# Performance work log

Measured on AMD Instinct MI355X. Metric: run time of the kernel, lower is better.

The kernel has to match this reference:

```python
import jax, jax.numpy as jnp
import numpy as np

T, B, D, H = 512, 64, 256, 512


def _linear_params(key, fan_in, fan_out, dtype=jnp.float32):
    # torch nn.Linear default init: U(-1/sqrt(fan_in), 1/sqrt(fan_in))
    k1, k2 = jax.random.split(key)
    bound = 1.0 / np.sqrt(fan_in)
    W = jax.random.uniform(k1, (fan_out, fan_in), dtype, -bound, bound)
    b = jax.random.uniform(k2, (fan_out,), dtype, -bound, bound)
    return W, b


def setup_inputs() -> dict:
    key = jax.random.key(0)
    kx, kf, ki, kg, ko = jax.random.split(key, 5)
    inputs = jax.random.normal(kx, (T, B, D), dtype=jnp.float32)
    Wf, bf = _linear_params(kf, D + H, H)
    Wi, bi = _linear_params(ki, D + H, H)
    Wg, bg = _linear_params(kg, D + H, H)
    Wo, bo = _linear_params(ko, D + H, H)
    return {"inputs": inputs, "Wf": Wf, "bf": bf, "Wi": Wi, "bi": bi,
            "Wg": Wg, "bg": bg, "Wo": Wo, "bo": bo}


def reference(inputs, Wf, bf, Wi, bi, Wg, bg, Wo, bo):
    # inputs: [T, B, D]; gate weights: [H, D+H]; biases: [H]
    batch = inputs.shape[1]
    hidden = Wf.shape[0]
    h0 = jnp.zeros((batch, hidden), dtype=inputs.dtype)
    c0 = jnp.zeros((batch, hidden), dtype=inputs.dtype)

    # Stack the 4 gate linears into one GEMM per step (same math).
    W_all = jnp.concatenate([Wf, Wi, Wg, Wo], axis=0)   # [4H, D+H]
    b_all = jnp.concatenate([bf, bi, bg, bo], axis=0)   # [4H]

    def step(carry, x):
        hx, cx = carry
        combined = jnp.concatenate([x, hx], axis=1)     # [B, D+H]
        gates = combined @ W_all.T + b_all              # [B, 4H]
        f, i, g, o = jnp.split(gates, 4, axis=1)
        f = jax.nn.sigmoid(f)
        i = jax.nn.sigmoid(i)
        g = jnp.tanh(g)
        o = jax.nn.sigmoid(o)
        cx = f * cx + i * g
        hx = o * jnp.tanh(cx)
        return (hx, cx), hx

    (hx, cx), outputs = jax.lax.scan(step, (h0, c0), inputs)
    return outputs, hx, cx
```

## Files before the change

kernel.cpp:

```cpp
#include <hip/hip_runtime.h>

static constexpr int T_STEPS = 512;
static constexpr int BATCH   = 64;
static constexpr int DIN     = 256;
static constexpr int HID     = 512;
static constexpr int KDIM    = DIN + HID;
static constexpr int S4      = 193;
static constexpr int NBLK    = 256;
static constexpr int NPROD   = 64;

__device__ __forceinline__ float fast_sigmoid(float v) {
    return 1.0f / (1.0f + __expf(-v));
}
__device__ __forceinline__ float fast_tanh(float v) {
    return 1.0f - 2.0f / (__expf(2.0f * v) + 1.0f);
}

__device__ __forceinline__ void store_bypass(float* p, float v) {
    __hip_atomic_store((unsigned int*)p, __float_as_uint(v),
                       __ATOMIC_RELAXED, __HIP_MEMORY_SCOPE_AGENT);
}
__device__ __forceinline__ float load_bypass(const float* p) {
    return __uint_as_float(__hip_atomic_load((const unsigned int*)p,
                           __ATOMIC_RELAXED, __HIP_MEMORY_SCOPE_AGENT));
}
__device__ __forceinline__ void store_flag(unsigned* p, unsigned v) {
    __hip_atomic_store(p, v, __ATOMIC_RELAXED, __HIP_MEMORY_SCOPE_AGENT);
}
__device__ __forceinline__ unsigned load_flag(const unsigned* p) {
    return __hip_atomic_load(p, __ATOMIC_RELAXED, __HIP_MEMORY_SCOPE_AGENT);
}

#define DPP_ADD(v, ctrl)                                                  \
    (v) += __uint_as_float(__builtin_amdgcn_update_dpp(                   \
        0u, __float_as_uint(v), (ctrl), 0xF, 0xF, true))

__global__ __launch_bounds__(512, 1)
void lstm_persistent(const float* __restrict__ x,
                     const float* __restrict__ Wf, const float* __restrict__ bfp,
                     const float* __restrict__ Wi, const float* __restrict__ bip,
                     const float* __restrict__ Wg, const float* __restrict__ bgp,
                     const float* __restrict__ Wo, const float* __restrict__ bop,
                     float* __restrict__ out, unsigned* __restrict__ flag_ws) {
    __shared__ float4 W4[32 * S4];
    __shared__ float4 C4[16 * S4];
    __shared__ float4 gates4[16 * 9];
    __shared__ float  bias_s[32];

    const int tid = threadIdx.x;
    const int wg  = blockIdx.x;
    const int bgroup = (wg & 7) >> 1;
    const int kslice = ((wg >> 3) << 1) | (wg & 1);
    const int bg0 = bgroup * 16;
    const int k0  = kslice * 8;

    unsigned* const flags = flag_ws + bgroup * NPROD;

    {
        const int r    = tid >> 4;
        const int c0   = tid & 15;
        const int gate = r >> 3;
        const int unit = k0 + (r & 7);
        const float* wsrc = (gate == 0) ? Wf : (gate == 1) ? Wi : (gate == 2) ? Wg : Wo;
        const float4* src4 = (const float4*)(wsrc + (size_t)unit * KDIM);
        #pragma unroll 2
        for (int m = 0; m < 12; ++m)
            W4[r * S4 + c0 + 16 * m] = src4[c0 + 16 * m];
        if (tid < 32) {
            const int g2 = tid >> 3;
            const float* bsrc = (g2 == 0) ? bfp : (g2 == 1) ? bip : (g2 == 2) ? bgp : bop;
            bias_s[tid] = bsrc[k0 + (tid & 7)];
        }
    }

    float* const hx_sec = out + (size_t)T_STEPS * BATCH * HID;
    float* const cx_sec = hx_sec + BATCH * HID;

    const int lb2 = tid >> 3;
    const int u2  = tid & 7;

    if (tid < 128)
        store_bypass(&hx_sec[(size_t)(bg0 + lb2) * HID + (k0 + u2)], 0.0f);
    __syncthreads();
    if (tid == 0)
        store_flag(&flags[kslice], 1u);

    const int kq  = tid & 31;
    const int rg  = (tid >> 5) & 7;
    const int lbg = tid >> 8;

    float c_reg = 0.0f;

    for (int t = 0; t < T_STEPS; ++t) {
        const float* h_read  = (t & 1) ? cx_sec : hx_sec;
        float*       h_write = (t & 1) ? hx_sec : cx_sec;

        {
            const float4* xs = (const float4*)(x + ((size_t)t * BATCH + bg0) * DIN);
            #pragma unroll
            for (int m = 0; m < 2; ++m) {
                const int i4 = tid + 512 * m;
                C4[(i4 >> 6) * S4 + (i4 & 63)] = xs[i4];
            }
        }
        __syncthreads();

        float acc[8][4];
        #pragma unroll
        for (int i = 0; i < 8; ++i)
            #pragma unroll
            for (int j = 0; j < 4; ++j) acc[i][j] = 0.0f;

        #pragma unroll 1
        for (int it = 0; it < 2; ++it) {
            const int dq = kq + 32 * it;
            float4 cv[8], wv[4];
            #pragma unroll
            for (int i = 0; i < 8; ++i) cv[i] = C4[(lbg * 8 + i) * S4 + dq];
            #pragma unroll
            for (int j = 0; j < 4; ++j) wv[j] = W4[(rg * 4 + j) * S4 + dq];
            #pragma unroll
            for (int i = 0; i < 8; ++i) {
                #pragma unroll
                for (int j = 0; j < 4; ++j) {
                    acc[i][j] = fmaf(cv[i].x, wv[j].x, acc[i][j]);
                    acc[i][j] = fmaf(cv[i].y, wv[j].y, acc[i][j]);
                    acc[i][j] = fmaf(cv[i].z, wv[j].z, acc[i][j]);
                    acc[i][j] = fmaf(cv[i].w, wv[j].w, acc[i][j]);
                }
            }
        }

        if (tid < 64) {
            const unsigned target = (unsigned)(t + 1);
            while (!__all((int)(load_flag(&flags[tid]) >= target)))
                __builtin_amdgcn_s_sleep(1);
        }
        __syncthreads();

        {
            const float* hsrc = h_read + (size_t)bg0 * HID;
            float hv[16];
            #pragma unroll
            for (int m = 0; m < 16; ++m)
                hv[m] = load_bypass(&hsrc[512 * m + tid]);
            float* Cf = (float*)C4;
            #pragma unroll
            for (int m = 0; m < 16; ++m)
                Cf[m * (S4 * 4) + 256 + tid] = hv[m];
        }
        __syncthreads();

        #pragma unroll 1
        for (int it = 2; it < 6; ++it) {
            const int dq = kq + 32 * it;
            float4 cv[8], wv[4];
            #pragma unroll
            for (int i = 0; i < 8; ++i) cv[i] = C4[(lbg * 8 + i) * S4 + dq];
            #pragma unroll
            for (int j = 0; j < 4; ++j) wv[j] = W4[(rg * 4 + j) * S4 + dq];
            #pragma unroll
            for (int i = 0; i < 8; ++i) {
                #pragma unroll
                for (int j = 0; j < 4; ++j) {
                    acc[i][j] = fmaf(cv[i].x, wv[j].x, acc[i][j]);
                    acc[i][j] = fmaf(cv[i].y, wv[j].y, acc[i][j]);
                    acc[i][j] = fmaf(cv[i].z, wv[j].z, acc[i][j]);
                    acc[i][j] = fmaf(cv[i].w, wv[j].w, acc[i][j]);
                }
            }
        }

        {
            const bool writer = ((tid & 31) == 16);
            #pragma unroll
            for (int i = 0; i < 8; ++i) {
                float g0, g1, g2, g3;
                {
                    float v = acc[i][0];
                    DPP_ADD(v, 0xB1); DPP_ADD(v, 0x4E);
                    DPP_ADD(v, 0x124); DPP_ADD(v, 0x128);
                    DPP_ADD(v, 0x142); g0 = v;
                }
                {
                    float v = acc[i][1];
                    DPP_ADD(v, 0xB1); DPP_ADD(v, 0x4E);
                    DPP_ADD(v, 0x124); DPP_ADD(v, 0x128);
                    DPP_ADD(v, 0x142); g1 = v;
                }
                {
                    float v = acc[i][2];
                    DPP_ADD(v, 0xB1); DPP_ADD(v, 0x4E);
                    DPP_ADD(v, 0x124); DPP_ADD(v, 0x128);
                    DPP_ADD(v, 0x142); g2 = v;
                }
                {
                    float v = acc[i][3];
                    DPP_ADD(v, 0xB1); DPP_ADD(v, 0x4E);
                    DPP_ADD(v, 0x124); DPP_ADD(v, 0x128);
                    DPP_ADD(v, 0x142); g3 = v;
                }
                if (writer)
                    gates4[(lbg * 8 + i) * 9 + rg] = make_float4(g0, g1, g2, g3);
            }
        }
        __syncthreads();

        if (tid < 128) {
            const float* gf = (const float*)gates4;
            const float pf = gf[lb2 * 36 + u2]      + bias_s[u2];
            const float pi = gf[lb2 * 36 + 8 + u2]  + bias_s[8 + u2];
            const float pg = gf[lb2 * 36 + 16 + u2] + bias_s[16 + u2];
            const float po = gf[lb2 * 36 + 24 + u2] + bias_s[24 + u2];
            const float fg = fast_sigmoid(pf);
            const float ig = fast_sigmoid(pi);
            const float gg = fast_tanh(pg);
            const float og = fast_sigmoid(po);
            c_reg = fg * c_reg + ig * gg;
            const float h = og * fast_tanh(c_reg);
            const int b = bg0 + lb2;
            const int k = k0 + u2;
            store_bypass(&h_write[(size_t)b * HID + k], h);
            out[((size_t)t * BATCH + b) * HID + k] = h;
        }
        __syncthreads();

        if (tid == 0)
            store_flag(&flags[kslice], (unsigned)(t + 2));
    }

    if (tid < 64) {
        const unsigned target = (unsigned)(T_STEPS + 1);
        while (!__all((int)(load_flag(&flags[tid]) >= target)))
            __builtin_amdgcn_s_sleep(1);
    }
    __syncthreads();
    if (tid < 128)
        cx_sec[(size_t)(bg0 + lb2) * HID + (k0 + u2)] = c_reg;
}

extern "C" void kernel_launch(void* const* d_in, const int* in_sizes, int n_in,
                              void* d_out, int out_size, void* d_ws, size_t ws_size,
                              hipStream_t stream) {
    (void)in_sizes; (void)n_in; (void)ws_size; (void)out_size;
    const float* x  = (const float*)d_in[0];
    const float* Wf = (const float*)d_in[1];
    const float* bf = (const float*)d_in[2];
    const float* Wi = (const float*)d_in[3];
    const float* bi = (const float*)d_in[4];
    const float* Wg = (const float*)d_in[5];
    const float* bg = (const float*)d_in[6];
    const float* Wo = (const float*)d_in[7];
    const float* bo = (const float*)d_in[8];
    float* out = (float*)d_out;
    unsigned* flags = (unsigned*)d_ws;

    hipMemsetAsync(d_ws, 0, 4 * NPROD * sizeof(unsigned), stream);

    void* args[] = {&x, &Wf, &bf, &Wi, &bi, &Wg, &bg, &Wo, &bo, &out, &flags};
    hipLaunchCooperativeKernel(reinterpret_cast<void*>(lstm_persistent),
                               dim3(NBLK), dim3(512), args, 0, stream);
}
```

Baseline: 2.658 ms.

## Re-tile per-step gate GEMM to 8x8 register tiles with wave-wide K reduction

Each thread now computes an 8-batch by 8-row register tile instead of 8x4, with 64 K-lanes per wave instead of 32. Each loaded activation vector is reused across twice as many weight rows, and the number of K-iterations drops from 6 to 3 (1 before the h wait, 2 after). The reduction gains one extra DPP step (row broadcast) to sum across the full 64-lane wave, and the writer lane is adjusted to match. Scheduling barriers are added between the weight-pair groups. The trade-off is twice as many accumulator registers, which may lower occupancy, and a different split of work between the overlapped x-part and the serial h-part.

```diff
diff --git a/kernel.cpp b/kernel.cpp
--- a/kernel.cpp
+++ b/kernel.cpp
@@ -85,9 +85,10 @@
     if (tid == 0)
         store_flag(&flags[kslice], 1u);
 
-    const int kq  = tid & 31;
-    const int rg  = (tid >> 5) & 7;
-    const int lbg = tid >> 8;
+    const int kq  = tid & 63;
+    const int wid = tid >> 6;
+    const int bg8 = (wid & 1) * 8;
+    const int rw  = (wid >> 1) * 8;
 
     float c_reg = 0.0f;
 
@@ -105,31 +106,36 @@
         }
         __syncthreads();
 
-        float acc[8][4];
+        float acc[8][8];
         #pragma unroll
         for (int i = 0; i < 8; ++i)
             #pragma unroll
-            for (int j = 0; j < 4; ++j) acc[i][j] = 0.0f;
-
-        #pragma unroll 1
-        for (int it = 0; it < 2; ++it) {
-            const int dq = kq + 32 * it;
-            float4 cv[8], wv[4];
-            #pragma unroll
-            for (int i = 0; i < 8; ++i) cv[i] = C4[(lbg * 8 + i) * S4 + dq];
-            #pragma unroll
-            for (int j = 0; j < 4; ++j) wv[j] = W4[(rg * 4 + j) * S4 + dq];
-            #pragma unroll
-            for (int i = 0; i < 8; ++i) {
+            for (int j = 0; j < 8; ++j) acc[i][j] = 0.0f;
+
+        auto gemm_kslice = [&](const int dq) {
+            float4 cv[8];
+            #pragma unroll
+            for (int i = 0; i < 8; ++i) cv[i] = C4[(bg8 + i) * S4 + dq];
+            #pragma unroll
+            for (int jp = 0; jp < 4; ++jp) {
+                const float4 w0 = W4[(rw + 2 * jp) * S4 + dq];
+                const float4 w1 = W4[(rw + 2 * jp + 1) * S4 + dq];
                 #pragma unroll
-                for (int j = 0; j < 4; ++j) {
-                    acc[i][j] = fmaf(cv[i].x, wv[j].x, acc[i][j]);
-                    acc[i][j] = fmaf(cv[i].y, wv[j].y, acc[i][j]);
-                    acc[i][j] = fmaf(cv[i].z, wv[j].z, acc[i][j]);
-                    acc[i][j] = fmaf(cv[i].w, wv[j].w, acc[i][j]);
+                for (int i = 0; i < 8; ++i) {
+                    acc[i][2 * jp]     = fmaf(cv[i].x, w0.x, acc[i][2 * jp]);
+                    acc[i][2 * jp]     = fmaf(cv[i].y, w0.y, acc[i][2 * jp]);
+                    acc[i][2 * jp]     = fmaf(cv[i].z, w0.z, acc[i][2 * jp]);
+                    acc[i][2 * jp]     = fmaf(cv[i].w, w0.w, acc[i][2 * jp]);
+                    acc[i][2 * jp + 1] = fmaf(cv[i].x, w1.x, acc[i][2 * jp + 1]);
+                    acc[i][2 * jp + 1] = fmaf(cv[i].y, w1.y, acc[i][2 * jp + 1]);
+                    acc[i][2 * jp + 1] = fmaf(cv[i].z, w1.z, acc[i][2 * jp + 1]);
+                    acc[i][2 * jp + 1] = fmaf(cv[i].w, w1.w, acc[i][2 * jp + 1]);
                 }
+                __builtin_amdgcn_sched_barrier(0);
             }
-        }
+        };
+
+        gemm_kslice(kq);
 
         if (tid < 64) {
             const unsigned target = (unsigned)(t + 1);
@@ -152,56 +158,28 @@
         __syncthreads();
 
         #pragma unroll 1
-        for (int it = 2; it < 6; ++it) {
-            const int dq = kq + 32 * it;
-            float4 cv[8], wv[4];
-            #pragma unroll
-            for (int i = 0; i < 8; ++i) cv[i] = C4[(lbg * 8 + i) * S4 + dq];
-            #pragma unroll
-            for (int j = 0; j < 4; ++j) wv[j] = W4[(rg * 4 + j) * S4 + dq];
+        for (int it = 1; it < 3; ++it)
+            gemm_kslice(kq + 64 * it);
+
+        {
+            const bool writer = (kq == 48);
             #pragma unroll
             for (int i = 0; i < 8; ++i) {
+                float g[8];
                 #pragma unroll
-                for (int j = 0; j < 4; ++j) {
-                    acc[i][j] = fmaf(cv[i].x, wv[j].x, acc[i][j]);
-                    acc[i][j] = fmaf(cv[i].y, wv[j].y, acc[i][j]);
-                    acc[i][j] = fmaf(cv[i].z, wv[j].z, acc[i][j]);
-                    acc[i][j] = fmaf(cv[i].w, wv[j].w, acc[i][j]);
+                for (int j = 0; j < 8; ++j) {
+                    float v = acc[i][j];
+                    DPP_ADD(v, 0xB1);  DPP_ADD(v, 0x4E);
+                    DPP_ADD(v, 0x124); DPP_ADD(v, 0x128);
+                    DPP_ADD(v, 0x142); DPP_ADD(v, 0x143);
+                    g[j] = v;
                 }
-            }
-        }
-
-        {
-            const bool writer = ((tid & 31) == 16);
-            #pragma unroll
-            for (int i = 0; i < 8; ++i) {
-                float g0, g1, g2, g3;
-                {
-                    float v = acc[i][0];
-                    DPP_ADD(v, 0xB1); DPP_ADD(v, 0x4E);
-                    DPP_ADD(v, 0x124); DPP_ADD(v, 0x128);
-                    DPP_ADD(v, 0x142); g0 = v;
+                if (writer) {
+                    gates4[(bg8 + i) * 9 + (rw >> 2)]     =
+                        make_float4(g[0], g[1], g[2], g[3]);
+                    gates4[(bg8 + i) * 9 + (rw >> 2) + 1] =
+                        make_float4(g[4], g[5], g[6], g[7]);
                 }
-                {
-                    float v = acc[i][1];
-                    DPP_ADD(v, 0xB1); DPP_ADD(v, 0x4E);
-                    DPP_ADD(v, 0x124); DPP_ADD(v, 0x128);
-                    DPP_ADD(v, 0x142); g1 = v;
-                }
-                {
-                    float v = acc[i][2];
-                    DPP_ADD(v, 0xB1); DPP_ADD(v, 0x4E);
-                    DPP_ADD(v, 0x124); DPP_ADD(v, 0x128);
-                    DPP_ADD(v, 0x142); g2 = v;
-                }
-                {
-                    float v = acc[i][3];
-                    DPP_ADD(v, 0xB1); DPP_ADD(v, 0x4E);
-                    DPP_ADD(v, 0x124); DPP_ADD(v, 0x128);
-                    DPP_ADD(v, 0x142); g3 = v;
-                }
-                if (writer)
-                    gates4[(lbg * 8 + i) * 9 + rg] = make_float4(g0, g1, g2, g3);
             }
         }
         __syncthreads();
```

Result: slower. 3.269 ms (+23.0%).

## Prefetch next-step input into shared memory and preload weights before spin-wait

Applied to the files above, without the earlier changes.

Moves the per-step load of x into shared memory so it happens after the gate reduction of the previous step, overlapping it with the activation phase and removing one barrier per step. It also preloads two weight slices into registers before the cross-block flag wait, so their LDS reads overlap with the synchronization latency. Address arithmetic is hoisted into precomputed base pointers. This adds register pressure, and correctness relies on the x region of C4 not being read by the activation phase when it is overwritten.

```diff
diff --git a/kernel.cpp b/kernel.cpp
--- a/kernel.cpp
+++ b/kernel.cpp
@@ -73,6 +73,15 @@
         }
     }
 
+    {
+        const float4* xs = (const float4*)(x + (size_t)bg0 * DIN);
+        #pragma unroll
+        for (int m = 0; m < 2; ++m) {
+            const int i4 = tid + 512 * m;
+            C4[(i4 >> 6) * S4 + (i4 & 63)] = xs[i4];
+        }
+    }
+
     float* const hx_sec = out + (size_t)T_STEPS * BATCH * HID;
     float* const cx_sec = hx_sec + BATCH * HID;
 
@@ -89,22 +98,15 @@
     const int rg  = (tid >> 5) & 7;
     const int lbg = tid >> 8;
 
+    const float4* const C4r = &C4[(lbg * 8) * S4 + kq];
+    const float4* const W4r = &W4[(rg * 4) * S4 + kq];
+
     float c_reg = 0.0f;
 
     for (int t = 0; t < T_STEPS; ++t) {
         const float* h_read  = (t & 1) ? cx_sec : hx_sec;
         float*       h_write = (t & 1) ? hx_sec : cx_sec;
 
-        {
-            const float4* xs = (const float4*)(x + ((size_t)t * BATCH + bg0) * DIN);
-            #pragma unroll
-            for (int m = 0; m < 2; ++m) {
-                const int i4 = tid + 512 * m;
-                C4[(i4 >> 6) * S4 + (i4 & 63)] = xs[i4];
-            }
-        }
-        __syncthreads();
-
         float acc[8][4];
         #pragma unroll
         for (int i = 0; i < 8; ++i)
@@ -113,12 +115,11 @@
 
         #pragma unroll 1
         for (int it = 0; it < 2; ++it) {
-            const int dq = kq + 32 * it;
             float4 cv[8], wv[4];
             #pragma unroll
-            for (int i = 0; i < 8; ++i) cv[i] = C4[(lbg * 8 + i) * S4 + dq];
-            #pragma unroll
-            for (int j = 0; j < 4; ++j) wv[j] = W4[(rg * 4 + j) * S4 + dq];
+            for (int i = 0; i < 8; ++i) cv[i] = C4r[i * S4 + 32 * it];
+            #pragma unroll
+            for (int j = 0; j < 4; ++j) wv[j] = W4r[j * S4 + 32 * it];
             #pragma unroll
             for (int i = 0; i < 8; ++i) {
                 #pragma unroll
@@ -131,6 +132,13 @@
             }
         }
 
+        float4 wp2[4], wp3[4];
+        #pragma unroll
+        for (int j = 0; j < 4; ++j) {
+            wp2[j] = W4r[j * S4 + 64];
+            wp3[j] = W4r[j * S4 + 96];
+        }
+
         if (tid < 64) {
             const unsigned target = (unsigned)(t + 1);
             while (!__all((int)(load_flag(&flags[tid]) >= target)))
@@ -152,13 +160,29 @@
         __syncthreads();
 
         #pragma unroll 1
-        for (int it = 2; it < 6; ++it) {
-            const int dq = kq + 32 * it;
+        for (int it = 2; it < 4; ++it) {
+            const float4* wp = (it == 2) ? wp2 : wp3;
+            float4 cv[8];
+            #pragma unroll
+            for (int i = 0; i < 8; ++i) cv[i] = C4r[i * S4 + 32 * it];
+            #pragma unroll
+            for (int i = 0; i < 8; ++i) {
+                #pragma unroll
+                for (int j = 0; j < 4; ++j) {
+                    acc[i][j] = fmaf(cv[i].x, wp[j].x, acc[i][j]);
+                    acc[i][j] = fmaf(cv[i].y, wp[j].y, acc[i][j]);
+                    acc[i][j] = fmaf(cv[i].z, wp[j].z, acc[i][j]);
+                    acc[i][j] = fmaf(cv[i].w, wp[j].w, acc[i][j]);
+                }
+            }
+        }
+        #pragma unroll 1
+        for (int it = 4; it < 6; ++it) {
             float4 cv[8], wv[4];
             #pragma unroll
-            for (int i = 0; i < 8; ++i) cv[i] = C4[(lbg * 8 + i) * S4 + dq];
-            #pragma unroll
-            for (int j = 0; j < 4; ++j) wv[j] = W4[(rg * 4 + j) * S4 + dq];
+            for (int i = 0; i < 8; ++i) cv[i] = C4r[i * S4 + 32 * it];
+            #pragma unroll
+            for (int j = 0; j < 4; ++j) wv[j] = W4r[j * S4 + 32 * it];
             #pragma unroll
             for (int i = 0; i < 8; ++i) {
                 #pragma unroll
@@ -206,6 +230,15 @@
         }
         __syncthreads();
 
+        {
+            const int tn = (t + 1 < T_STEPS) ? (t + 1) : t;
+            const float4* xs = (const float4*)(x + ((size_t)tn * BATCH + bg0) * DIN);
+            #pragma unroll
+            for (int m = 0; m < 2; ++m) {
+                const int i4 = tid + 512 * m;
+                C4[(i4 >> 6) * S4 + (i4 & 63)] = xs[i4];
+            }
+        }
         if (tid < 128) {
             const float* gf = (const float*)gates4;
             const float pf = gf[lb2 * 36 + u2]      + bias_s[u2];
```

Result: slower. 2.763 ms (+4.0%).

## Apply gate nonlinearities in registers and prefetch next-step input

Applied to the files above, without the earlier changes.

Weight rows are reordered so each row group holds the four gates of one hidden unit. The reduced gate sums can then be consumed directly in registers by owner lanes, which removes the shared gates buffer and one block barrier per step. The x tile for the next step is loaded after the current GEMM, removing the barrier at the top of each step. Bias values are hoisted into registers and LDS addressing is simplified; the cost is more divergent select logic and the next-step x load landing on the critical path before the flag publish.

```diff
diff --git a/kernel.cpp b/kernel.cpp
--- a/kernel.cpp
+++ b/kernel.cpp
@@ -44,7 +44,6 @@
                      float* __restrict__ out, unsigned* __restrict__ flag_ws) {
     __shared__ float4 W4[32 * S4];
     __shared__ float4 C4[16 * S4];
-    __shared__ float4 gates4[16 * 9];
     __shared__ float  bias_s[32];
 
     const int tid = threadIdx.x;
@@ -59,28 +58,34 @@
     {
         const int r    = tid >> 4;
         const int c0   = tid & 15;
-        const int gate = r >> 3;
-        const int unit = k0 + (r & 7);
+        const int gate = r & 3;
+        const int unit = k0 + (r >> 2);
         const float* wsrc = (gate == 0) ? Wf : (gate == 1) ? Wi : (gate == 2) ? Wg : Wo;
         const float4* src4 = (const float4*)(wsrc + (size_t)unit * KDIM);
         #pragma unroll 2
         for (int m = 0; m < 12; ++m)
             W4[r * S4 + c0 + 16 * m] = src4[c0 + 16 * m];
         if (tid < 32) {
-            const int g2 = tid >> 3;
+            const int g2 = tid & 3;
             const float* bsrc = (g2 == 0) ? bfp : (g2 == 1) ? bip : (g2 == 2) ? bgp : bop;
-            bias_s[tid] = bsrc[k0 + (tid & 7)];
+            bias_s[tid] = bsrc[k0 + (tid >> 2)];
+        }
+    }
+
+    {
+        const float4* xs = (const float4*)(x + (size_t)bg0 * DIN);
+        #pragma unroll
+        for (int m = 0; m < 2; ++m) {
+            const int i4 = tid + 512 * m;
+            C4[(i4 >> 6) * S4 + (i4 & 63)] = xs[i4];
         }
     }
 
     float* const hx_sec = out + (size_t)T_STEPS * BATCH * HID;
     float* const cx_sec = hx_sec + BATCH * HID;
 
-    const int lb2 = tid >> 3;
-    const int u2  = tid & 7;
-
     if (tid < 128)
-        store_bypass(&hx_sec[(size_t)(bg0 + lb2) * HID + (k0 + u2)], 0.0f);
+        store_bypass(&hx_sec[(size_t)(bg0 + (tid >> 3)) * HID + (k0 + (tid & 7))], 0.0f);
     __syncthreads();
     if (tid == 0)
         store_flag(&flags[kslice], 1u);
@@ -89,22 +94,25 @@
     const int rg  = (tid >> 5) & 7;
     const int lbg = tid >> 8;
 
+    const float4* const C4r = &C4[(lbg * 8) * S4 + kq];
+    const float4* const W4r = &W4[(rg * 4) * S4 + kq];
+
+    const int  sub   = tid & 31;
+    const bool owner = (sub >= 16) && (sub < 24);
+    const int  ob    = bg0 + lbg * 8 + (sub - 16);
+    const int  ok    = k0 + rg;
+
+    const float bb0 = bias_s[rg * 4 + 0];
+    const float bb1 = bias_s[rg * 4 + 1];
+    const float bb2 = bias_s[rg * 4 + 2];
+    const float bb3 = bias_s[rg * 4 + 3];
+
     float c_reg = 0.0f;
 
     for (int t = 0; t < T_STEPS; ++t) {
         const float* h_read  = (t & 1) ? cx_sec : hx_sec;
         float*       h_write = (t & 1) ? hx_sec : cx_sec;
 
-        {
-            const float4* xs = (const float4*)(x + ((size_t)t * BATCH + bg0) * DIN);
-            #pragma unroll
-            for (int m = 0; m < 2; ++m) {
-                const int i4 = tid + 512 * m;
-                C4[(i4 >> 6) * S4 + (i4 & 63)] = xs[i4];
-            }
-        }
-        __syncthreads();
-
         float acc[8][4];
         #pragma unroll
         for (int i = 0; i < 8; ++i)
@@ -113,12 +121,11 @@
 
         #pragma unroll 1
         for (int it = 0; it < 2; ++it) {
-            const int dq = kq + 32 * it;
             float4 cv[8], wv[4];
             #pragma unroll
-            for (int i = 0; i < 8; ++i) cv[i] = C4[(lbg * 8 + i) * S4 + dq];
-            #pragma unroll
-            for (int j = 0; j < 4; ++j) wv[j] = W4[(rg * 4 + j) * S4 + dq];
+            for (int i = 0; i < 8; ++i) cv[i] = C4r[i * S4 + 32 * it];
+            #pragma unroll
+            for (int j = 0; j < 4; ++j) wv[j] = W4r[j * S4 + 32 * it];
             #pragma unroll
             for (int i = 0; i < 8; ++i) {
                 #pragma unroll
@@ -153,12 +160,11 @@
 
         #pragma unroll 1
         for (int it = 2; it < 6; ++it) {
-            const int dq = kq + 32 * it;
             float4 cv[8], wv[4];
             #pragma unroll
-            for (int i = 0; i < 8; ++i) cv[i] = C4[(lbg * 8 + i) * S4 + dq];
-            #pragma unroll
-            for (int j = 0; j < 4; ++j) wv[j] = W4[(rg * 4 + j) * S4 + dq];
+            for (int i = 0; i < 8; ++i) cv[i] = C4r[i * S4 + 32 * it];
+            #pragma unroll
+            for (int j = 0; j < 4; ++j) wv[j] = W4r[j * S4 + 32 * it];
             #pragma unroll
             for (int i = 0; i < 8; ++i) {
                 #pragma unroll
@@ -172,56 +178,55 @@
         }
 
         {
-            const bool writer = ((tid & 31) == 16);
-            #pragma unroll
-            for (int i = 0; i < 8; ++i) {
-                float g0, g1, g2, g3;
-                {
-                    float v = acc[i][0];
-                    DPP_ADD(v, 0xB1); DPP_ADD(v, 0x4E);
-                    DPP_ADD(v, 0x124); DPP_ADD(v, 0x128);
-                    DPP_ADD(v, 0x142); g0 = v;
-                }
-                {
-                    float v = acc[i][1];
-                    DPP_ADD(v, 0xB1); DPP_ADD(v, 0x4E);
-                    DPP_ADD(v, 0x124); DPP_ADD(v, 0x128);
-                    DPP_ADD(v, 0x142); g1 = v;
-                }
-                {
-                    float v = acc[i][2];
-                    DPP_ADD(v, 0xB1); DPP_ADD(v, 0x4E);
-                    DPP_ADD(v, 0x124); DPP_ADD(v, 0x128);
-                    DPP_ADD(v, 0x142); g2 = v;
-                }
-                {
-                    float v = acc[i][3];
-                    DPP_ADD(v, 0xB1); DPP_ADD(v, 0x4E);
-                    DPP_ADD(v, 0x124); DPP_ADD(v, 0x128);
-                    DPP_ADD(v, 0x142); g3 = v;
-                }
-                if (writer)
-                    gates4[(lbg * 8 + i) * 9 + rg] = make_float4(g0, g1, g2, g3);
-            }
-        }
-        __syncthreads();
-
-        if (tid < 128) {
-            const float* gf = (const float*)gates4;
-            const float pf = gf[lb2 * 36 + u2]      + bias_s[u2];
-            const float pi = gf[lb2 * 36 + 8 + u2]  + bias_s[8 + u2];
-            const float pg = gf[lb2 * 36 + 16 + u2] + bias_s[16 + u2];
-            const float po = gf[lb2 * 36 + 24 + u2] + bias_s[24 + u2];
-            const float fg = fast_sigmoid(pf);
-            const float ig = fast_sigmoid(pi);
-            const float gg = fast_tanh(pg);
-            const float og = fast_sigmoid(po);
+            const int tn = (t + 1 < T_STEPS) ? (t + 1) : t;
+            const float4* xs = (const float4*)(x + ((size_t)tn * BATCH + bg0) * DIN);
+            #pragma unroll
+            for (int m = 0; m < 2; ++m) {
+                const int i4 = tid + 512 * m;
+                C4[(i4 >> 6) * S4 + (i4 & 63)] = xs[i4];
+            }
+        }
+
+        float pf = 0.0f, pi = 0.0f, pg = 0.0f, po = 0.0f;
+        #pragma unroll
+        for (int i = 0; i < 8; ++i) {
+            float g0, g1, g2, g3;
+            {
+                float v = acc[i][0];
+                DPP_ADD(v, 0xB1); DPP_ADD(v, 0x4E);
+                DPP_ADD(v, 0x124); DPP_ADD(v, 0x128);
+                DPP_ADD(v, 0x142); g0 = v;
+            }
+            {
+                float v = acc[i][1];
+                DPP_ADD(v, 0xB1); DPP_ADD(v, 0x4E);
+                DPP_ADD(v, 0x124); DPP_ADD(v, 0x128);
+                DPP_ADD(v, 0x142); g1 = v;
+            }
+            {
+                float v = acc[i][2];
+                DPP_ADD(v, 0xB1); DPP_ADD(v, 0x4E);
+                DPP_ADD(v, 0x124); DPP_ADD(v, 0x128);
+                DPP_ADD(v, 0x142); g2 = v;
+            }
+            {
+                float v = acc[i][3];
+                DPP_ADD(v, 0xB1); DPP_ADD(v, 0x4E);
+                DPP_ADD(v, 0x124); DPP_ADD(v, 0x128);
+                DPP_ADD(v, 0x142); g3 = v;
+            }
+            if (sub == 16 + i) { pf = g0; pi = g1; pg = g2; po = g3; }
+        }
+
+        if (owner) {
+            const float fg = fast_sigmoid(pf + bb0);
+            const float ig = fast_sigmoid(pi + bb1);
+            const float gg = fast_tanh(pg + bb2);
+            const float og = fast_sigmoid(po + bb3);
             c_reg = fg * c_reg + ig * gg;
             const float h = og * fast_tanh(c_reg);
-            const int b = bg0 + lb2;
-            const int k = k0 + u2;
-            store_bypass(&h_write[(size_t)b * HID + k], h);
-            out[((size_t)t * BATCH + b) * HID + k] = h;
+            store_bypass(&h_write[(size_t)ob * HID + ok], h);
+            out[((size_t)t * BATCH + ob) * HID + ok] = h;
         }
         __syncthreads();
 
@@ -235,8 +240,8 @@
             __builtin_amdgcn_s_sleep(1);
     }
     __syncthreads();
-    if (tid < 128)
-        cx_sec[(size_t)(bg0 + lb2) * HID + (k0 + u2)] = c_reg;
+    if (owner)
+        cx_sec[(size_t)ob * HID + ok] = c_reg;
 }
 
 extern "C" void kernel_launch(void* const* d_in, const int* in_sizes, int n_in,
```

Measured after the change: 2.696 ms. Within noise of the previous version (+1.4%).
